# Kernel tuning notes

Measured on AMD Instinct MI355X. Metric: run time of the kernel, lower is better.

## Reference

```python
import jax, jax.numpy as jnp
import numpy as np

B, N, D, E, H = 16, 256, 64, 64, 8


def setup_inputs() -> dict:
    key = jax.random.key(0)
    ks = jax.random.split(key, 16)
    s = 0.05
    return {
        "query": jax.random.normal(ks[0], (B, N, D), jnp.float32),
        "edges_augmented": jax.random.normal(ks[1], (B, N, N, E), jnp.float32),
        "Wq": jax.random.normal(ks[2], (D, H * D), jnp.float32) * s,
        "bq": jnp.zeros((H * D,), jnp.float32),
        "Wk": jax.random.normal(ks[3], (D, H * D), jnp.float32) * s,
        "bk": jnp.zeros((H * D,), jnp.float32),
        "Wv": jax.random.normal(ks[4], (D, H * D), jnp.float32) * s,
        "bv": jnp.zeros((H * D,), jnp.float32),
        "Wa": jax.random.normal(ks[5], (E, H), jnp.float32) * s,
        "ba": jnp.zeros((H,), jnp.float32),
        "Wg": jax.random.normal(ks[6], (E, H), jnp.float32) * s,
        "bg": jnp.zeros((H,), jnp.float32),
        "Wo": jax.random.normal(ks[7], (H * D, D), jnp.float32) * s,
        "bo": jnp.zeros((D,), jnp.float32),
        "We": jax.random.normal(ks[8], (H, E), jnp.float32) * s,
        "be": jnp.zeros((E,), jnp.float32),
    }


def reference(query, edges_augmented, Wq, bq, Wk, bk, Wv, bv, Wa, ba, Wg, bg, Wo, bo, We, be):
    b, n, d = query.shape
    h = Wa.shape[1]
    # QKV projections -> [b, h, n, d]
    Q = (query @ Wq + bq).reshape(b, n, h, d).transpose(0, 2, 1, 3)
    Kt = (query @ Wk + bk).reshape(b, n, h, d).transpose(0, 2, 1, 3)
    V = (query @ Wv + bv).reshape(b, n, h, d).transpose(0, 2, 1, 3)
    scores = jnp.einsum('bhnd,bhmd->bhnm', Q, Kt) / jnp.sqrt(jnp.asarray(d, query.dtype))
    # edge-derived additive bias: [b,n,n,h] -> [b,h,n,n]
    attn_bias = (edges_augmented @ Wa + ba).transpose(0, 3, 1, 2)
    scores = scores + attn_bias
    # sigmoid gate on values
    g = jax.nn.sigmoid((edges_augmented @ Wg + bg).transpose(0, 3, 1, 2))  # [b,h,n,n]
    Vg = jnp.einsum('bhnm,bhmd->bhnd', g, V)
    attn = jax.nn.softmax(scores, axis=-1)
    out = jnp.einsum('bhnm,bhmd->bhnd', attn, Vg)
    out = out.transpose(0, 2, 1, 3).reshape(b, n, h * d)
    attention_output = out @ Wo + bo  # [b, n, d]
    # edges output: scores [b,h,n,m] -> [b,m,n,h] -> Dense to E
    edges_output = scores.transpose(0, 3, 2, 1) @ We + be  # [b, n, n, E]
    return (attention_output, edges_output)
```

## Files before the change

kernel.cpp:

```cpp
#include <hip/hip_runtime.h>

#define BB 16
#define NN 256
#define DD 64
#define EE 64
#define HH 8

typedef __attribute__((ext_vector_type(4))) float f32x4;
typedef __attribute__((ext_vector_type(8))) short short8;

__device__ __forceinline__ void fma4(float* acc, float x, float4 w) {
    acc[0] += x * w.x; acc[1] += x * w.y; acc[2] += x * w.z; acc[3] += x * w.w;
}

__device__ __forceinline__ unsigned short f2bf(float f) {
    union { float f; unsigned u; } v; v.f = f;
    unsigned r = v.u + 0x7FFFu + ((v.u >> 16) & 1u);
    return (unsigned short)(r >> 16);
}

__global__ __launch_bounds__(256) void qkv_kernel(
    const float* __restrict__ query,
    const float* __restrict__ Wq, const float* __restrict__ bq,
    const float* __restrict__ Wk, const float* __restrict__ bk,
    const float* __restrict__ Wv, const float* __restrict__ bv,
    unsigned short* __restrict__ Qb, unsigned short* __restrict__ Kb,
    unsigned short* __restrict__ Vtb)
{
    __shared__ __align__(16) float q_l[8][64];
    const int mtx = blockIdx.x >> 9;
    const int rem = blockIdx.x & 511;
    const int b   = rem >> 5;
    const int n0  = (rem & 31) << 3;
    const int tid = threadIdx.x;

    if (tid < 128)
        ((float4*)&q_l[0][0])[tid] =
            ((const float4*)(query + (size_t)(b * NN + n0) * DD))[tid];

    const int w    = tid >> 6;
    const int lane = tid & 63;
    const int r0   = w * 2;
    const float* W  = (mtx == 0) ? Wq : (mtx == 1) ? Wk : Wv;
    const float* bs = (mtx == 0) ? bq : (mtx == 1) ? bk : bv;

    const int c0 = lane << 2;
    float acc[2][2][4];
    {
        const float4 b0 = *(const float4*)(bs + c0);
        const float4 b1 = *(const float4*)(bs + 256 + c0);
        acc[0][0][0]=b0.x; acc[0][0][1]=b0.y; acc[0][0][2]=b0.z; acc[0][0][3]=b0.w;
        acc[0][1][0]=b1.x; acc[0][1][1]=b1.y; acc[0][1][2]=b1.z; acc[0][1][3]=b1.w;
        acc[1][0][0]=b0.x; acc[1][0][1]=b0.y; acc[1][0][2]=b0.z; acc[1][0][3]=b0.w;
        acc[1][1][0]=b1.x; acc[1][1][1]=b1.y; acc[1][1][2]=b1.z; acc[1][1][3]=b1.w;
    }
    __syncthreads();

    #pragma unroll 2
    for (int d4 = 0; d4 < 16; ++d4) {
        const float4 qa = ((const float4*)&q_l[r0][0])[d4];
        const float4 qb = ((const float4*)&q_l[r0 + 1][0])[d4];
        const float qav[4] = {qa.x, qa.y, qa.z, qa.w};
        const float qbv[4] = {qb.x, qb.y, qb.z, qb.w};
        #pragma unroll
        for (int k = 0; k < 4; ++k) {
            const float4 w0 = *(const float4*)(W + (size_t)(d4 * 4 + k) * 512 + c0);
            const float4 w1 = *(const float4*)(W + (size_t)(d4 * 4 + k) * 512 + 256 + c0);
            fma4(acc[0][0], qav[k], w0); fma4(acc[0][1], qav[k], w1);
            fma4(acc[1][0], qbv[k], w0); fma4(acc[1][1], qbv[k], w1);
        }
    }

    const int hq = lane >> 4;
    const int d0 = (lane & 15) << 2;
    if (mtx < 2) {
        unsigned short* T = (mtx == 0) ? Qb : Kb;
        const float scale = (mtx == 0) ? 0.125f : 1.0f;
        #pragma unroll
        for (int r = 0; r < 2; ++r)
            #pragma unroll
            for (int j = 0; j < 2; ++j) {
                const int h = j * 4 + hq;
                const unsigned int lo = (unsigned)f2bf(acc[r][j][0] * scale)
                                      | ((unsigned)f2bf(acc[r][j][1] * scale) << 16);
                const unsigned int hi = (unsigned)f2bf(acc[r][j][2] * scale)
                                      | ((unsigned)f2bf(acc[r][j][3] * scale) << 16);
                uint2* p = (uint2*)(T + ((size_t)(b * HH + h) * NN + n0 + r0 + r) * DD + d0);
                *p = make_uint2(lo, hi);
            }
    } else {
        #pragma unroll
        for (int r = 0; r < 2; ++r)
            #pragma unroll
            for (int j = 0; j < 2; ++j) {
                const int h = j * 4 + hq;
                #pragma unroll
                for (int k = 0; k < 4; ++k)
                    Vtb[((size_t)(b * HH + h) * DD + d0 + k) * NN + n0 + r0 + r] =
                        f2bf(acc[r][j][k]);
            }
    }
}

__global__ __launch_bounds__(256) void qk_kernel(
    const unsigned short* __restrict__ Qb, const unsigned short* __restrict__ Kb,
    float* __restrict__ scores)
{
    const int bh = blockIdx.x >> 3;
    const int nt = (blockIdx.x >> 1) & 3;
    const int mh = blockIdx.x & 1;
    const int tid = threadIdx.x;
    const int w = tid >> 6, l = tid & 63;
    const int lr = l & 15, lg = l >> 4;
    const int n0 = nt * 64 + w * 16;

    const unsigned short* qp = Qb + ((size_t)bh * NN + n0 + lr) * DD + lg * 8;
    const unsigned short* kp = Kb + ((size_t)bh * NN + mh * 128 + lr) * DD + lg * 8;

    const short8 a0 = *(const short8*)qp;
    const short8 a1 = *(const short8*)(qp + 32);

    f32x4 acc[8];
    #pragma unroll
    for (int mt = 0; mt < 8; ++mt) acc[mt] = (f32x4){0.f, 0.f, 0.f, 0.f};

    #pragma unroll
    for (int mt = 0; mt < 8; ++mt) {
        const short8 b0 = *(const short8*)(kp + (size_t)mt * 16 * DD);
        const short8 b1 = *(const short8*)(kp + (size_t)mt * 16 * DD + 32);
        acc[mt] = __builtin_amdgcn_mfma_f32_16x16x32_bf16(a0, b0, acc[mt], 0, 0, 0);
        acc[mt] = __builtin_amdgcn_mfma_f32_16x16x32_bf16(a1, b1, acc[mt], 0, 0, 0);
    }

    float* sp = scores + (size_t)bh * NN * NN;
    #pragma unroll
    for (int mt = 0; mt < 8; ++mt)
        #pragma unroll
        for (int r = 0; r < 4; ++r)
            sp[(size_t)(n0 + lg * 4 + r) * NN + mh * 128 + mt * 16 + lr] = acc[mt][r];
}

__global__ __launch_bounds__(256) void edges_kernel(
    const float* __restrict__ edges,
    const float* __restrict__ Wa, const float* __restrict__ ba,
    const float* __restrict__ Wg, const float* __restrict__ bg,
    const float* __restrict__ We, const float* __restrict__ be,
    float* __restrict__ scores,
    unsigned short* __restrict__ gates,
    float* __restrict__ edges_out)
{
    __shared__ __align__(16) unsigned short eb[128 * 64];
    __shared__ __align__(16) unsigned short wc[16 * 64];
    __shared__ float bgl[128][17];
    __shared__ float bal[8], bgb[8];

    const int mh  = blockIdx.x & 1;
    const int n   = (blockIdx.x >> 1) & 255;
    const int b   = blockIdx.x >> 9;
    const int m0  = mh << 7;
    const int tid = threadIdx.x;
    const int w   = tid >> 6, l = tid & 63;
    const int lr  = l & 15, lg = l >> 4;

    float wecol[8];
    #pragma unroll
    for (int h = 0; h < 8; ++h) wecol[h] = We[h * EE + l];
    const float bev = be[l];

    #pragma unroll
    for (int j = 0; j < 4; ++j) {
        const int idx = tid * 4 + j;
        const int hp = idx >> 6, e = idx & 63;
        const float v = (hp < 8) ? Wa[e * 8 + hp] : Wg[e * 8 + (hp - 8)];
        *(unsigned short*)((char*)wc + hp * 128 + ((e * 2) ^ ((hp & 7) << 4))) = f2bf(v);
    }
    if (tid < 8) { bal[tid] = ba[tid]; bgb[tid] = bg[tid]; }

    const float4* esrc = (const float4*)(edges + ((size_t)(b * NN + n) * NN + m0) * DD);
    #pragma unroll
    for (int it = 0; it < 8; ++it) {
        const int c = it * 256 + tid;
        const float4 x = esrc[c];
        const int m = c >> 4, e4 = c & 15;
        const unsigned lo = (unsigned)f2bf(x.x) | ((unsigned)f2bf(x.y) << 16);
        const unsigned hi = (unsigned)f2bf(x.z) | ((unsigned)f2bf(x.w) << 16);
        *(uint2*)((char*)eb + m * 128 + ((e4 * 8) ^ ((m & 7) << 4))) = make_uint2(lo, hi);
    }
    __syncthreads();

    short8 bfrag[2];
    #pragma unroll
    for (int ks = 0; ks < 2; ++ks)
        bfrag[ks] = *(const short8*)((char*)wc + lr * 128 +
                                     ((ks * 64 + lg * 16) ^ ((lr & 7) << 4)));

    #pragma unroll
    for (int t = 0; t < 2; ++t) {
        const int T = w * 2 + t;
        f32x4 acc = (f32x4){0.f, 0.f, 0.f, 0.f};
        #pragma unroll
        for (int ks = 0; ks < 2; ++ks) {
            const int m = T * 16 + lr;
            const short8 af = *(const short8*)((char*)eb + m * 128 +
                                 ((ks * 64 + lg * 16) ^ ((lr & 7) << 4)));
            acc = __builtin_amdgcn_mfma_f32_16x16x32_bf16(af, bfrag[ks], acc, 0, 0, 0);
        }
        #pragma unroll
        for (int r = 0; r < 4; ++r)
            bgl[T * 16 + lg * 4 + r][lr] = acc[r];
    }
    __syncthreads();

    {
        const int m  = tid & 127;
        const int hh = tid >> 7;
        #pragma unroll
        for (int i = 0; i < 4; ++i) {
            const int h = hh * 4 + i;
            const size_t off = ((size_t)(b * HH + h) << 16) + (n << 8) + m0 + m;
            const float sc = scores[off] + bgl[m][h] + bal[h];
            scores[off] = sc;
            bgl[m][h]   = sc;
            const float gv = bgl[m][8 + h] + bgb[h];
            gates[off] = f2bf(1.f / (1.f + __expf(-gv)));
        }
    }
    __syncthreads();

    #pragma unroll 4
    for (int mi = 0; mi < 32; ++mi) {
        const int m = w * 32 + mi;
        float v = bev;
        #pragma unroll
        for (int h = 0; h < 8; ++h) v += bgl[m][h] * wecol[h];
        edges_out[((size_t)(b * NN + m0 + m) * NN + n) * DD + l] = v;
    }
}

__global__ __launch_bounds__(256) void vg_kernel(
    const unsigned short* __restrict__ gates, const unsigned short* __restrict__ Vtb,
    unsigned short* __restrict__ Vgt)
{
    const int bh = blockIdx.x >> 2;
    const int q  = blockIdx.x & 3;
    const int tid = threadIdx.x;
    const int w = tid >> 6, l = tid & 63;
    const int lr = l & 15, lg = l >> 4;
    const int n0 = q * 64 + w * 16;

    const unsigned short* gp = gates + ((size_t)bh * NN + n0 + lr) * NN + lg * 8;
    const unsigned short* vp = Vtb + ((size_t)bh * DD + lr) * NN + lg * 8;

    f32x4 acc[4];
    #pragma unroll
    for (int dt = 0; dt < 4; ++dt) acc[dt] = (f32x4){0.f, 0.f, 0.f, 0.f};

    #pragma unroll
    for (int ks = 0; ks < 8; ++ks) {
        const short8 bfr = *(const short8*)(gp + ks * 32);
        #pragma unroll
        for (int dt = 0; dt < 4; ++dt) {
            const short8 afr = *(const short8*)(vp + (size_t)dt * 16 * NN + ks * 32);
            acc[dt] = __builtin_amdgcn_mfma_f32_16x16x32_bf16(afr, bfr, acc[dt], 0, 0, 0);
        }
    }

    unsigned short* op = Vgt + (size_t)bh * DD * NN;
    #pragma unroll
    for (int dt = 0; dt < 4; ++dt)
        #pragma unroll
        for (int r = 0; r < 4; ++r)
            op[(size_t)(dt * 16 + lg * 4 + r) * NN + n0 + lr] = f2bf(acc[dt][r]);
}

__global__ __launch_bounds__(512) void out_kernel(
    const float* __restrict__ scores, const unsigned short* __restrict__ Vgt,
    const float* __restrict__ Wo, const float* __restrict__ bo,
    float* __restrict__ att_out)
{
    __shared__ float o_l[16][521];
    const int b  = blockIdx.x >> 4;
    const int nt = blockIdx.x & 15;
    const int n0 = nt * 16;
    const int tid = threadIdx.x;
    const int w = tid >> 6, l = tid & 63;
    const int lr = l & 15, lg = l >> 4;
    const int h = w;

    {
        const float* sp = scores + ((size_t)(b * HH + h) * NN + n0 + lr) * NN + lg * 8;
        float s[64];
        #pragma unroll
        for (int ks = 0; ks < 8; ++ks) {
            const float4 x0 = *(const float4*)(sp + ks * 32);
            const float4 x1 = *(const float4*)(sp + ks * 32 + 4);
            s[ks * 8 + 0] = x0.x; s[ks * 8 + 1] = x0.y;
            s[ks * 8 + 2] = x0.z; s[ks * 8 + 3] = x0.w;
            s[ks * 8 + 4] = x1.x; s[ks * 8 + 5] = x1.y;
            s[ks * 8 + 6] = x1.z; s[ks * 8 + 7] = x1.w;
        }
        float mx = -1e30f;
        #pragma unroll
        for (int i = 0; i < 64; ++i) mx = fmaxf(mx, s[i]);
        mx = fmaxf(mx, __shfl_xor(mx, 16, 64));
        mx = fmaxf(mx, __shfl_xor(mx, 32, 64));
        float sm = 0.f;
        #pragma unroll
        for (int i = 0; i < 64; ++i) { s[i] = __expf(s[i] - mx); sm += s[i]; }
        sm += __shfl_xor(sm, 16, 64);
        sm += __shfl_xor(sm, 32, 64);
        const float inv = 1.f / sm;

        const unsigned short* vp = Vgt + ((size_t)(b * HH + h) * DD + lr) * NN + lg * 8;
        f32x4 acc[4];
        #pragma unroll
        for (int dt = 0; dt < 4; ++dt) acc[dt] = (f32x4){0.f, 0.f, 0.f, 0.f};

        #pragma unroll
        for (int ks = 0; ks < 8; ++ks) {
            union { short8 v; unsigned short u[8]; } bf;
            #pragma unroll
            for (int j = 0; j < 8; ++j) bf.u[j] = f2bf(s[ks * 8 + j] * inv);
            #pragma unroll
            for (int dt = 0; dt < 4; ++dt) {
                const short8 afr = *(const short8*)(vp + (size_t)dt * 16 * NN + ks * 32);
                acc[dt] = __builtin_amdgcn_mfma_f32_16x16x32_bf16(afr, bf.v, acc[dt], 0, 0, 0);
            }
        }
        #pragma unroll
        for (int dt = 0; dt < 4; ++dt)
            #pragma unroll
            for (int r = 0; r < 4; ++r)
                o_l[lr][h * 64 + dt * 16 + lg * 4 + r] = acc[dt][r];
    }
    __syncthreads();

    const int n  = tid >> 5;
    const int d2 = (tid & 31) << 1;
    float a0 = bo[d2], a1 = bo[d2 + 1];
    const float* orow = &o_l[n][0];
    #pragma unroll 8
    for (int k = 0; k < 512; ++k) {
        const float o = orow[k];
        const float2 w2 = *(const float2*)(Wo + (size_t)k * 64 + d2);
        a0 += o * w2.x; a1 += o * w2.y;
    }
    *(float2*)(att_out + ((size_t)(b * NN + n0 + n)) * DD + d2) = make_float2(a0, a1);
}

extern "C" void kernel_launch(void* const* d_in, const int* in_sizes, int n_in,
                              void* d_out, int out_size, void* d_ws, size_t ws_size,
                              hipStream_t stream)
{
    const float* query = (const float*)d_in[0];
    const float* edges = (const float*)d_in[1];
    const float* Wq = (const float*)d_in[2];  const float* bq = (const float*)d_in[3];
    const float* Wk = (const float*)d_in[4];  const float* bk = (const float*)d_in[5];
    const float* Wv = (const float*)d_in[6];  const float* bv = (const float*)d_in[7];
    const float* Wa = (const float*)d_in[8];  const float* ba = (const float*)d_in[9];
    const float* Wg = (const float*)d_in[10]; const float* bg = (const float*)d_in[11];
    const float* Wo = (const float*)d_in[12]; const float* bo = (const float*)d_in[13];
    const float* We = (const float*)d_in[14]; const float* be = (const float*)d_in[15];

    float* att_out   = (float*)d_out;
    float* edges_out = (float*)d_out + 262144;

    char* base = (char*)d_ws;
    float*          scores = (float*)base;
    unsigned short* gates  = (unsigned short*)(base + 33554432);
    unsigned short* Qb     = (unsigned short*)(base + 50331648);
    unsigned short* Kb     = (unsigned short*)(base + 54525952);
    unsigned short* Vtb    = (unsigned short*)(base + 58720256);
    unsigned short* Vgt    = (unsigned short*)(base + 62914560);

    hipLaunchKernelGGL(qkv_kernel, dim3(1536), dim3(256), 0, stream,
                       query, Wq, bq, Wk, bk, Wv, bv, Qb, Kb, Vtb);
    hipLaunchKernelGGL(qk_kernel, dim3(1024), dim3(256), 0, stream,
                       Qb, Kb, scores);
    hipLaunchKernelGGL(edges_kernel, dim3(8192), dim3(256), 0, stream,
                       edges, Wa, ba, Wg, bg, We, be, scores, gates, edges_out);
    hipLaunchKernelGGL(vg_kernel, dim3(512), dim3(256), 0, stream,
                       gates, Vtb, Vgt);
    hipLaunchKernelGGL(out_kernel, dim3(256), dim3(512), 0, stream,
                       scores, Vgt, Wo, bo, att_out);
}
```

Baseline: 588.8 us.

## Add nontemporal loads/stores, hoist score load, vectorize LDS reads, split vg grid

```diff
diff --git a/kernel.cpp b/kernel.cpp
--- a/kernel.cpp
+++ b/kernel.cpp
@@ -151,7 +151,7 @@
 {
     __shared__ __align__(16) unsigned short eb[128 * 64];
     __shared__ __align__(16) unsigned short wc[16 * 64];
-    __shared__ float bgl[128][17];
+    __shared__ __align__(16) float bgl[128][20];
     __shared__ float bal[8], bgb[8];
 
     const int mh  = blockIdx.x & 1;
@@ -161,6 +161,13 @@
     const int tid = threadIdx.x;
     const int w   = tid >> 6, l = tid & 63;
     const int lr  = l & 15, lg = l >> 4;
+
+    const int fm = tid & 127;
+    const int fh = (tid >> 7) << 2;
+    const size_t so0 = ((size_t)(b * HH + fh) << 16) + ((size_t)n << 8) + m0 + fm;
+    float qk[4];
+    #pragma unroll
+    for (int i = 0; i < 4; ++i) qk[i] = scores[so0 + ((size_t)i << 16)];
 
     float wecol[8];
     #pragma unroll
@@ -176,14 +183,14 @@
     }
     if (tid < 8) { bal[tid] = ba[tid]; bgb[tid] = bg[tid]; }
 
-    const float4* esrc = (const float4*)(edges + ((size_t)(b * NN + n) * NN + m0) * DD);
+    const f32x4* esrc = (const f32x4*)(edges + ((size_t)(b * NN + n) * NN + m0) * DD);
     #pragma unroll
     for (int it = 0; it < 8; ++it) {
         const int c = it * 256 + tid;
-        const float4 x = esrc[c];
+        const f32x4 x = __builtin_nontemporal_load(esrc + c);
         const int m = c >> 4, e4 = c & 15;
-        const unsigned lo = (unsigned)f2bf(x.x) | ((unsigned)f2bf(x.y) << 16);
-        const unsigned hi = (unsigned)f2bf(x.z) | ((unsigned)f2bf(x.w) << 16);
+        const unsigned lo = (unsigned)f2bf(x[0]) | ((unsigned)f2bf(x[1]) << 16);
+        const unsigned hi = (unsigned)f2bf(x[2]) | ((unsigned)f2bf(x[3]) << 16);
         *(uint2*)((char*)eb + m * 128 + ((e4 * 8) ^ ((m & 7) << 4))) = make_uint2(lo, hi);
     }
     __syncthreads();
@@ -211,29 +218,27 @@
     }
     __syncthreads();
 
-    {
-        const int m  = tid & 127;
-        const int hh = tid >> 7;
-        #pragma unroll
-        for (int i = 0; i < 4; ++i) {
-            const int h = hh * 4 + i;
-            const size_t off = ((size_t)(b * HH + h) << 16) + (n << 8) + m0 + m;
-            const float sc = scores[off] + bgl[m][h] + bal[h];
-            scores[off] = sc;
-            bgl[m][h]   = sc;
-            const float gv = bgl[m][8 + h] + bgb[h];
-            gates[off] = f2bf(1.f / (1.f + __expf(-gv)));
-        }
+    #pragma unroll
+    for (int i = 0; i < 4; ++i) {
+        const int h = fh + i;
+        const float sc = qk[i] + bgl[fm][h] + bal[h];
+        scores[so0 + ((size_t)i << 16)] = sc;
+        bgl[fm][h] = sc;
+        const float gv = bgl[fm][8 + h] + bgb[h];
+        gates[so0 + ((size_t)i << 16)] = f2bf(1.f / (1.f + __expf(-gv)));
     }
     __syncthreads();
 
     #pragma unroll 4
     for (int mi = 0; mi < 32; ++mi) {
         const int m = w * 32 + mi;
-        float v = bev;
-        #pragma unroll
-        for (int h = 0; h < 8; ++h) v += bgl[m][h] * wecol[h];
-        edges_out[((size_t)(b * NN + m0 + m) * NN + n) * DD + l] = v;
+        const float4 sa = *(const float4*)&bgl[m][0];
+        const float4 sb = *(const float4*)&bgl[m][4];
+        const float v = bev
+            + sa.x * wecol[0] + sa.y * wecol[1] + sa.z * wecol[2] + sa.w * wecol[3]
+            + sb.x * wecol[4] + sb.y * wecol[5] + sb.z * wecol[6] + sb.w * wecol[7];
+        __builtin_nontemporal_store(v,
+            edges_out + ((size_t)(b * NN + m0 + m) * NN + n) * DD + l);
     }
 }
 
@@ -241,8 +246,9 @@
     const unsigned short* __restrict__ gates, const unsigned short* __restrict__ Vtb,
     unsigned short* __restrict__ Vgt)
 {
-    const int bh = blockIdx.x >> 2;
-    const int q  = blockIdx.x & 3;
+    const int dh = blockIdx.x & 1;
+    const int q  = (blockIdx.x >> 1) & 3;
+    const int bh = blockIdx.x >> 3;
     const int tid = threadIdx.x;
     const int w = tid >> 6, l = tid & 63;
     const int lr = l & 15, lg = l >> 4;
@@ -251,26 +257,26 @@
     const unsigned short* gp = gates + ((size_t)bh * NN + n0 + lr) * NN + lg * 8;
     const unsigned short* vp = Vtb + ((size_t)bh * DD + lr) * NN + lg * 8;
 
-    f32x4 acc[4];
-    #pragma unroll
-    for (int dt = 0; dt < 4; ++dt) acc[dt] = (f32x4){0.f, 0.f, 0.f, 0.f};
+    f32x4 acc[2];
+    #pragma unroll
+    for (int dt = 0; dt < 2; ++dt) acc[dt] = (f32x4){0.f, 0.f, 0.f, 0.f};
 
     #pragma unroll
     for (int ks = 0; ks < 8; ++ks) {
         const short8 bfr = *(const short8*)(gp + ks * 32);
         #pragma unroll
-        for (int dt = 0; dt < 4; ++dt) {
-            const short8 afr = *(const short8*)(vp + (size_t)dt * 16 * NN + ks * 32);
+        for (int dt = 0; dt < 2; ++dt) {
+            const short8 afr = *(const short8*)(vp + (size_t)(dh * 2 + dt) * 16 * NN + ks * 32);
             acc[dt] = __builtin_amdgcn_mfma_f32_16x16x32_bf16(afr, bfr, acc[dt], 0, 0, 0);
         }
     }
 
     unsigned short* op = Vgt + (size_t)bh * DD * NN;
     #pragma unroll
-    for (int dt = 0; dt < 4; ++dt)
+    for (int dt = 0; dt < 2; ++dt)
         #pragma unroll
         for (int r = 0; r < 4; ++r)
-            op[(size_t)(dt * 16 + lg * 4 + r) * NN + n0 + lr] = f2bf(acc[dt][r]);
+            op[(size_t)((dh * 2 + dt) * 16 + lg * 4 + r) * NN + n0 + lr] = f2bf(acc[dt][r]);
 }
 
 __global__ __launch_bounds__(512) void out_kernel(
@@ -288,16 +294,17 @@
     const int h = w;
 
     {
-        const float* sp = scores + ((size_t)(b * HH + h) * NN + n0 + lr) * NN + lg * 8;
+        const f32x4* sp = (const f32x4*)(scores +
+            ((size_t)(b * HH + h) * NN + n0 + lr) * NN + lg * 8);
         float s[64];
         #pragma unroll
         for (int ks = 0; ks < 8; ++ks) {
-            const float4 x0 = *(const float4*)(sp + ks * 32);
-            const float4 x1 = *(const float4*)(sp + ks * 32 + 4);
-            s[ks * 8 + 0] = x0.x; s[ks * 8 + 1] = x0.y;
-            s[ks * 8 + 2] = x0.z; s[ks * 8 + 3] = x0.w;
-            s[ks * 8 + 4] = x1.x; s[ks * 8 + 5] = x1.y;
-            s[ks * 8 + 6] = x1.z; s[ks * 8 + 7] = x1.w;
+            const f32x4 x0 = __builtin_nontemporal_load(sp + ks * 8);
+            const f32x4 x1 = __builtin_nontemporal_load(sp + ks * 8 + 1);
+            s[ks * 8 + 0] = x0[0]; s[ks * 8 + 1] = x0[1];
+            s[ks * 8 + 2] = x0[2]; s[ks * 8 + 3] = x0[3];
+            s[ks * 8 + 4] = x1[0]; s[ks * 8 + 5] = x1[1];
+            s[ks * 8 + 6] = x1[2]; s[ks * 8 + 7] = x1[3];
         }
         float mx = -1e30f;
         #pragma unroll
@@ -379,7 +386,7 @@
                        Qb, Kb, scores);
     hipLaunchKernelGGL(edges_kernel, dim3(8192), dim3(256), 0, stream,
                        edges, Wa, ba, Wg, bg, We, be, scores, gates, edges_out);
-    hipLaunchKernelGGL(vg_kernel, dim3(512), dim3(256), 0, stream,
+    hipLaunchKernelGGL(vg_kernel, dim3(1024), dim3(256), 0, stream,
                        gates, Vtb, Vgt);
     hipLaunchKernelGGL(out_kernel, dim3(256), dim3(512), 0, stream,
                        scores, Vgt, Wo, bo, att_out);
```

Result: faster. 575.8 us (-2.2%).
